# Kernel tuning notes

Hardware: AMD Instinct MI355X
Metric: run time of the kernel (lower is better)

## Reference

```python
import jax, jax.numpy as jnp
import numpy as np
from functools import partial

H = 51

def lstm_cell(x, h, c, W_ih, W_hh, b_ih, b_hh):
    # PyTorch LSTMCell: gates ordered (i, f, g, o)
    z = x @ W_ih.T + b_ih + h @ W_hh.T + b_hh  # [B, 4H]
    i, f, g, o = jnp.split(z, 4, axis=-1)
    i = jax.nn.sigmoid(i)
    f = jax.nn.sigmoid(f)
    g = jnp.tanh(g)
    o = jax.nn.sigmoid(o)
    c_new = f * c + i * g
    h_new = o * jnp.tanh(c_new)
    return h_new, c_new


def setup_inputs() -> dict:
    key = jax.random.key(0)
    ks = jax.random.split(key, 12)
    B, T = 2048, 512
    s = 1.0 / np.sqrt(H)  # PyTorch default init scale
    inp = {
        "input": jax.random.normal(ks[0], (B, T), dtype=jnp.float32),
        "W_ih1": jax.random.uniform(ks[1], (4 * H, 1), jnp.float32, -s, s),
        "W_hh1": jax.random.uniform(ks[2], (4 * H, H), jnp.float32, -s, s),
        "b_ih1": jax.random.uniform(ks[3], (4 * H,), jnp.float32, -s, s),
        "b_hh1": jax.random.uniform(ks[4], (4 * H,), jnp.float32, -s, s),
        "W_ih2": jax.random.uniform(ks[5], (4 * H, H), jnp.float32, -s, s),
        "W_hh2": jax.random.uniform(ks[6], (4 * H, H), jnp.float32, -s, s),
        "b_ih2": jax.random.uniform(ks[7], (4 * H,), jnp.float32, -s, s),
        "b_hh2": jax.random.uniform(ks[8], (4 * H,), jnp.float32, -s, s),
        "W_lin": jax.random.uniform(ks[9], (1, H), jnp.float32, -s, s),
        "b_lin": jax.random.uniform(ks[10], (1,), jnp.float32, -s, s),
        "future": 32,
    }
    return inp


def reference(input, W_ih1, W_hh1, b_ih1, b_hh1, W_ih2, W_hh2, b_ih2, b_hh2, W_lin, b_lin, future):
    B, T = input.shape
    dt = input.dtype
    h1 = jnp.zeros((B, H), dt)
    c1 = jnp.zeros((B, H), dt)
    h2 = jnp.zeros((B, H), dt)
    c2 = jnp.zeros((B, H), dt)

    def core(carry, x_t):
        h1, c1, h2, c2 = carry
        h1, c1 = lstm_cell(x_t, h1, c1, W_ih1, W_hh1, b_ih1, b_hh1)
        h2, c2 = lstm_cell(h1, h2, c2, W_ih2, W_hh2, b_ih2, b_hh2)
        out = h2 @ W_lin.T + b_lin  # [B, 1]
        return (h1, c1, h2, c2), out

    xs = input.T[:, :, None]  # [T, B, 1]
    carry, outs = jax.lax.scan(core, (h1, c1, h2, c2), xs)

    def fstep(carry, _):
        state, out = carry
        new_state, new_out = core(state, out)
        return (new_state, new_out), new_out

    last_out = outs[-1]
    _, fouts = jax.lax.scan(fstep, (carry, last_out), None, length=future)

    all_outs = jnp.concatenate([outs, fouts], axis=0)  # [T+future, B, 1]
    return all_outs[:, :, 0].T  # [B, T+future]
```

## Files before the change

### kernel.cpp

```cpp
#include <hip/hip_runtime.h>

#define H 51
#define TIN 512
#define TTOT 544
#define BTILE 8
#define AST 88
#define H2ST 13
#define SOST 548
#define NTHR 768
#define NSLOT 3

typedef __attribute__((ext_vector_type(8))) short short8;
typedef __attribute__((ext_vector_type(4))) float float4v;

#define MFMA __builtin_amdgcn_mfma_f32_16x16x32_bf16

__device__ __forceinline__ float fast_rcp(float x) { return __builtin_amdgcn_rcpf(x); }
__device__ __forceinline__ float sigf(float x)  { return fast_rcp(1.0f + __expf(-x)); }
__device__ __forceinline__ float tanhf_(float x){ return 1.0f - 2.0f * fast_rcp(1.0f + __expf(2.0f * x)); }

__device__ __forceinline__ unsigned short bf16rnd(float x) {
    unsigned int u = __float_as_uint(x);
    return (unsigned short)((u + 0x7fffu + ((u >> 16) & 1u)) >> 16);
}
__device__ __forceinline__ unsigned int bf16pk(float a, float b) {
    unsigned int r;
    asm("v_cvt_pk_bf16_f32 %0, %1, %2" : "=v"(r) : "v"(a), "v"(b));
    return r;
}
__device__ __forceinline__ void bf16split(float x, unsigned short& hi, float& lo) {
    unsigned int u  = __float_as_uint(x);
    unsigned int hr = (u + 0x7fffu + ((u >> 16) & 1u)) & 0xffff0000u;
    hi = (unsigned short)(hr >> 16);
    lo = x - __uint_as_float(hr);
}

__device__ __forceinline__ float b1val(int k, int u, int g,
                                       const float* Whh1, const float* Wih1) {
    if (u >= H) return 0.0f;
    const int r = g * H + u;
    if (k < H)  return Whh1[r * H + k];
    if (k == H) return Wih1[r];
    return 0.0f;
}
__device__ __forceinline__ float b2val(int k, int u, int g,
                                       const float* Wih2, const float* Whh2) {
    if (u >= H) return 0.0f;
    const int r = g * H + u;
    if (k < H) return Wih2[r * H + k];
    if (k >= 64 && k < 64 + H) return Whh2[r * H + (k - 64)];
    return 0.0f;
}

__global__ __launch_bounds__(NTHR)
__attribute__((amdgpu_waves_per_eu(3, 3)))
void lstm_seq(
    const float* __restrict__ input,
    const float* __restrict__ W_ih1,
    const float* __restrict__ W_hh1,
    const float* __restrict__ b_ih1,
    const float* __restrict__ b_hh1,
    const float* __restrict__ W_ih2,
    const float* __restrict__ W_hh2,
    const float* __restrict__ b_ih2,
    const float* __restrict__ b_hh2,
    const float* __restrict__ W_lin,
    const float* __restrict__ b_lin,
    float* __restrict__ out)
{
    __shared__ __align__(16) unsigned short sA1h[NSLOT][16][AST];
    __shared__ __align__(16) unsigned short sA2h[NSLOT][16][AST];
    __shared__ float sH2f[NSLOT][64][H2ST];
    __shared__ __align__(8) float sXlo[NSLOT][8];
    __shared__ float sWlin[64];
    __shared__ __align__(16) float sIn[BTILE][TIN];
    __shared__ __align__(16) float sOut[BTILE][SOST];
    __shared__ int sCnt[4];

    const int tid  = threadIdx.x;
    const int lane = tid & 63;
    const int wv   = tid >> 6;
    const int ut   = wv & 3;
    const int quad = lane >> 4;
    const int kq   = quad * 8;
    const int nl   = lane & 15;
    const int u    = ut * 16 + nl;
    const int ur   = (u < H) ? u : (H - 1);
    const int b0   = blockIdx.x * BTILE;
    const float blin = b_lin[0];
    const int rowA = (quad & 1) * 4 + (quad >> 1) * 2;
    const int arow = quad * 4;
    const int kc   = lane & 31;
    const int bhead= 2 * ut + (lane >> 5);

    volatile int* vc = (volatile int*)sCnt;
    auto spin = [&](int idx, int v) __attribute__((always_inline)) {
        while (vc[idx] < v) __builtin_amdgcn_s_sleep(1);
        asm volatile("" ::: "memory");
    };
    auto bump = [&](int idx) __attribute__((always_inline)) {
        asm volatile("s_waitcnt lgkmcnt(0)" ::: "memory");
        if (lane == 0) atomicAdd(&sCnt[idx], 1);
    };

    {
        unsigned short* p0 = &sA1h[0][0][0];
        unsigned short* p2 = &sA2h[0][0][0];
        for (int i = tid; i < NSLOT * 16 * AST; i += NTHR) { p0[i] = 0; p2[i] = 0; }
        float* pf = &sH2f[0][0][0];
        for (int i = tid; i < NSLOT * 64 * H2ST; i += NTHR) pf[i] = 0.0f;
        if (tid < NSLOT * 8) sXlo[tid >> 3][tid & 7] = 0.0f;
        if (tid < 64) sWlin[tid] = (tid < H) ? W_lin[tid] : 0.0f;
        if (tid == 0) { sCnt[0] = 0; sCnt[1] = 4; sCnt[2] = 0; }
        for (int i = tid; i < BTILE * (TIN / 4); i += NTHR) {
            const int r = i >> 7, c = i & 127;
            *(float4v*)&sIn[r][c * 4] =
                *(const float4v*)&input[(size_t)(b0 + r) * TIN + c * 4];
        }
    }
    __syncthreads();
    if (tid < 8) {
        unsigned short hh; float lo;
        bf16split(sIn[tid][0], hh, lo);
        sA1h[0][(tid & 2) ? tid + 6 : tid][51] = hh;
        sXlo[0][tid] = lo;
    }
    __syncthreads();

    if (wv < 4) {
        short8 B1h[4][2];
        float zb1[4], wxf[4];
        #pragma unroll
        for (int g = 0; g < 4; ++g) {
            #pragma unroll
            for (int kt = 0; kt < 2; ++kt)
                #pragma unroll
                for (int j = 0; j < 8; ++j)
                    B1h[g][kt][j] = (short)bf16rnd(b1val(kt * 32 + kq + j, u, g, W_hh1, W_ih1));
            const int r = g * H + ur;
            zb1[g] = b_ih1[r] + b_hh1[r];
            wxf[g] = W_ih1[r];
        }
        float c1[2] = {0, 0};

        auto l1work = [&](int rs, int ws) __attribute__((always_inline)) {
            short8 a0h = *(const short8*)&sA1h[rs][nl][kq];
            short8 a1h = *(const short8*)&sA1h[rs][nl][32 + kq];
            float2 xl = *(const float2*)&sXlo[rs][rowA];
            float4v C[4];
            #pragma unroll
            for (int g = 0; g < 4; ++g) {
                float4v c = {zb1[g], zb1[g], zb1[g], zb1[g]};
                c = MFMA(a0h, B1h[g][0], c, 0, 0, 0);
                c = MFMA(a1h, B1h[g][1], c, 0, 0, 0);
                C[g] = c;
            }
            float h1v[2];
            #pragma unroll
            for (int j = 0; j < 2; ++j) {
                const float xr = j ? xl.y : xl.x;
                float I = sigf  (C[0][j] + wxf[0] * xr);
                float F = sigf  (C[1][j] + wxf[1] * xr);
                float G = tanhf_(C[2][j] + wxf[2] * xr);
                float O = sigf  (C[3][j] + wxf[3] * xr);
                c1[j] = F * c1[j] + I * G;
                h1v[j] = O * tanhf_(c1[j]);
            }
            if (u < H) {
                const unsigned int pk = bf16pk(h1v[0], h1v[1]);
                sA1h[ws][arow][u]     = (unsigned short)pk;
                sA1h[ws][arow + 1][u] = (unsigned short)(pk >> 16);
            }
        };

        {
            int si = 0, so = 1, t1 = 0;
            for (int s = 0; s < TIN; ++s) {
                spin(0, t1); spin(2, t1); spin(1, t1 - 4);
                l1work(si, so);
                bump(0);
                t1 += 4;
                si = so; so = (so == 2) ? 0 : so + 1;
            }
        }
        __syncthreads();
        for (int s = TIN; s <= TTOT; ++s) {
            const int rs = s % 3, ws = (s + 1) % 3;
            __syncthreads();
            __syncthreads();
            if (s < TTOT) l1work(rs, ws);
            __syncthreads();
        }
    } else if (wv < 8) {
        short8 B2h[4][4];
        float zb2[4];
        #pragma unroll
        for (int g = 0; g < 4; ++g) {
            #pragma unroll
            for (int kt = 0; kt < 4; ++kt)
                #pragma unroll
                for (int j = 0; j < 8; ++j)
                    B2h[g][kt][j] = (short)bf16rnd(b2val(kt * 32 + kq + j, u, g, W_ih2, W_hh2));
            const int r = g * H + ur;
            zb2[g] = b_ih2[r] + b_hh2[r];
        }
        float c2[2] = {0, 0};

        auto l2work = [&](int rs, int ws) __attribute__((always_inline)) {
            short8 f0h = *(const short8*)&sA1h[rs][nl][kq];
            short8 f1h = *(const short8*)&sA1h[rs][nl][32 + kq];
            short8 f2h = *(const short8*)&sA2h[rs][nl][kq];
            short8 f3h = *(const short8*)&sA2h[rs][nl][32 + kq];
            float4v C[4];
            #pragma unroll
            for (int g = 0; g < 4; ++g) {
                float4v c = {zb2[g], zb2[g], zb2[g], zb2[g]};
                c = MFMA(f0h, B2h[g][0], c, 0, 0, 0);
                c = MFMA(f1h, B2h[g][1], c, 0, 0, 0);
                c = MFMA(f2h, B2h[g][2], c, 0, 0, 0);
                c = MFMA(f3h, B2h[g][3], c, 0, 0, 0);
                C[g] = c;
            }
            float h2v[2];
            #pragma unroll
            for (int j = 0; j < 2; ++j) {
                float I = sigf  (C[0][j]);
                float F = sigf  (C[1][j]);
                float G = tanhf_(C[2][j]);
                float O = sigf  (C[3][j]);
                c2[j] = F * c2[j] + I * G;
                h2v[j] = O * tanhf_(c2[j]);
            }
            if (u < H) {
                const unsigned int pk = bf16pk(h2v[0], h2v[1]);
                sA2h[ws][arow][u]     = (unsigned short)pk;
                sA2h[ws][arow + 1][u] = (unsigned short)(pk >> 16);
                sH2f[rs][u][rowA]     = h2v[0];
                sH2f[rs][u][rowA + 1] = h2v[1];
            }
        };

        {
            int si = 1, so = 2, t4 = 4;
            for (int t = 1; t < TIN; ++t) {
                spin(0, t4); spin(1, t4); spin(2, t4 - 4);
                l2work(si, so);
                bump(1);
                t4 += 4;
                si = so; so = (so == 2) ? 0 : so + 1;
            }
        }
        __syncthreads();
        for (int s = TIN; s <= TTOT; ++s) {
            const int rs = s % 3, ws = (s + 1) % 3;
            l2work(rs, ws);
            __syncthreads();
            __syncthreads();
            __syncthreads();
        }
    } else {
        auto headw = [&](int slot, int outt) __attribute__((always_inline)) -> float {
            float p = sWlin[kc]      * sH2f[slot][kc][bhead]
                    + sWlin[kc + 32] * sH2f[slot][kc + 32][bhead];
            p += __shfl_xor(p, 1);  p += __shfl_xor(p, 2);  p += __shfl_xor(p, 4);
            p += __shfl_xor(p, 8);  p += __shfl_xor(p, 16);
            float val = p + blin;
            if (kc == 0) sOut[bhead][outt] = val;
            return val;
        };

        {
            int sm1 = 2, so = 1, t4 = 0;
            for (int s = 0; s < TIN; ++s) {
                spin(0, t4 - 4);
                if (s >= 2) { spin(1, t4); headw(sm1, s - 2); }
                if ((wv == 8) && (lane < 8) && (s + 1 < TIN)) {
                    unsigned short hh; float lo; bf16split(sIn[lane][s + 1], hh, lo);
                    sA1h[so][(lane & 2) ? lane + 6 : lane][51] = hh;
                    sXlo[so][lane] = lo;
                }
                bump(2);
                t4 += 4;
                sm1 = (sm1 == 2) ? 0 : sm1 + 1;
                so  = (so  == 2) ? 0 : so + 1;
            }
        }
        __syncthreads();
        for (int s = TIN; s <= TTOT; ++s) {
            const int rs = s % 3;
            __syncthreads();
            {
                float val = headw(rs, s - 1);
                if (kc == 0 && s < TTOT) {
                    unsigned short hh; float lo; bf16split(val, hh, lo);
                    sA1h[rs][(bhead & 2) ? bhead + 6 : bhead][51] = hh;
                    sXlo[rs][bhead] = lo;
                }
                if (s == TIN) headw((TIN - 1) % 3, s - 2);
            }
            __syncthreads();
            __syncthreads();
        }
    }

    __syncthreads();
    for (int i = tid; i < BTILE * (TTOT / 4); i += NTHR) {
        const int r = i / (TTOT / 4);
        const int c = i - r * (TTOT / 4);
        *(float4v*)&out[(size_t)(b0 + r) * TTOT + c * 4] =
            *(const float4v*)&sOut[r][c * 4];
    }
}

extern "C" void kernel_launch(void* const* d_in, const int* in_sizes, int n_in,
                              void* d_out, int out_size, void* d_ws, size_t ws_size,
                              hipStream_t stream) {
    const float* input = (const float*)d_in[0];
    const float* W_ih1 = (const float*)d_in[1];
    const float* W_hh1 = (const float*)d_in[2];
    const float* b_ih1 = (const float*)d_in[3];
    const float* b_hh1 = (const float*)d_in[4];
    const float* W_ih2 = (const float*)d_in[5];
    const float* W_hh2 = (const float*)d_in[6];
    const float* b_ih2 = (const float*)d_in[7];
    const float* b_hh2 = (const float*)d_in[8];
    const float* W_lin = (const float*)d_in[9];
    const float* b_lin = (const float*)d_in[10];
    float* out = (float*)d_out;

    lstm_seq<<<dim3(256), dim3(NTHR), 0, stream>>>(input, W_ih1, W_hh1, b_ih1, b_hh1,
                                                   W_ih2, W_hh2, b_ih2, b_hh2,
                                                   W_lin, b_lin, out);
}
```

Baseline: 469.8 us.

## Replace barrier-driven future phase with counter spin-waits and combined three-counter polling

The future-prediction phase (autoregressive steps after the input sequence) now uses the same shared-memory counter handshake as the main loop instead of three or four __syncthreads per step. The slot rotation and counter thresholds are reworked so all three wave groups (layer 1, layer 2, head) proceed in a pipelined fashion throughout. The per-counter spin with s_sleep is replaced by one loop that polls all three counters without sleeping. This cuts barrier overhead and wakeup latency, at the cost of busier polling that competes for LDS bandwidth and issue slots, and a higher risk of ordering bugs in the reworked slot and threshold logic.

```diff
diff --git a/kernel.cpp b/kernel.cpp
--- a/kernel.cpp
+++ b/kernel.cpp
@@ -94,8 +94,11 @@
     const int bhead= 2 * ut + (lane >> 5);
 
     volatile int* vc = (volatile int*)sCnt;
-    auto spin = [&](int idx, int v) __attribute__((always_inline)) {
-        while (vc[idx] < v) __builtin_amdgcn_s_sleep(1);
+    auto spin3 = [&](int v1, int v2, int vA) __attribute__((always_inline)) {
+        for (;;) {
+            int a = vc[0], b = vc[1], c = vc[2];
+            if (a >= v1 && b >= v2 && c >= vA) break;
+        }
         asm volatile("" ::: "memory");
     };
     auto bump = [&](int idx) __attribute__((always_inline)) {
@@ -111,7 +114,7 @@
         for (int i = tid; i < NSLOT * 64 * H2ST; i += NTHR) pf[i] = 0.0f;
         if (tid < NSLOT * 8) sXlo[tid >> 3][tid & 7] = 0.0f;
         if (tid < 64) sWlin[tid] = (tid < H) ? W_lin[tid] : 0.0f;
-        if (tid == 0) { sCnt[0] = 0; sCnt[1] = 4; sCnt[2] = 0; }
+        if (tid == 0) { sCnt[0] = 0; sCnt[1] = 0; sCnt[2] = 0; }
         for (int i = tid; i < BTILE * (TIN / 4); i += NTHR) {
             const int r = i >> 7, c = i & 127;
             *(float4v*)&sIn[r][c * 4] =
@@ -122,8 +125,8 @@
     if (tid < 8) {
         unsigned short hh; float lo;
         bf16split(sIn[tid][0], hh, lo);
-        sA1h[0][(tid & 2) ? tid + 6 : tid][51] = hh;
-        sXlo[0][tid] = lo;
+        sA1h[2][(tid & 2) ? tid + 6 : tid][51] = hh;
+        sXlo[2][tid] = lo;
     }
     __syncthreads();
 
@@ -174,22 +177,21 @@
         };
 
         {
-            int si = 0, so = 1, t1 = 0;
+            int rs = 2, ws = 0;
             for (int s = 0; s < TIN; ++s) {
-                spin(0, t1); spin(2, t1); spin(1, t1 - 4);
-                l1work(si, so);
+                const int t4 = 4 * s;
+                spin3(t4, t4 - 8, t4);
+                l1work(rs, ws);
                 bump(0);
-                t1 += 4;
-                si = so; so = (so == 2) ? 0 : so + 1;
-            }
-        }
-        __syncthreads();
-        for (int s = TIN; s <= TTOT; ++s) {
-            const int rs = s % 3, ws = (s + 1) % 3;
-            __syncthreads();
-            __syncthreads();
-            if (s < TTOT) l1work(rs, ws);
-            __syncthreads();
+                rs = ws; ws = (ws == 2) ? 0 : ws + 1;
+            }
+            for (int s = TIN; s < TTOT; ++s) {
+                const int t4 = 4 * s;
+                spin3(t4, t4 - 8, t4 + 4);
+                l1work(rs, ws);
+                bump(0);
+                rs = ws; ws = (ws == 2) ? 0 : ws + 1;
+            }
         }
     } else if (wv < 8) {
         short8 B2h[4][4];
@@ -235,28 +237,27 @@
                 const unsigned int pk = bf16pk(h2v[0], h2v[1]);
                 sA2h[ws][arow][u]     = (unsigned short)pk;
                 sA2h[ws][arow + 1][u] = (unsigned short)(pk >> 16);
-                sH2f[rs][u][rowA]     = h2v[0];
-                sH2f[rs][u][rowA + 1] = h2v[1];
+                sH2f[ws][u][rowA]     = h2v[0];
+                sH2f[ws][u][rowA + 1] = h2v[1];
             }
         };
 
         {
-            int si = 1, so = 2, t4 = 4;
-            for (int t = 1; t < TIN; ++t) {
-                spin(0, t4); spin(1, t4); spin(2, t4 - 4);
-                l2work(si, so);
+            int rs = 0, ws = 1;
+            for (int k = 1; k < TIN; ++k) {
+                const int t4 = 4 * k;
+                spin3(t4, t4 - 4, t4);
+                l2work(rs, ws);
                 bump(1);
-                t4 += 4;
-                si = so; so = (so == 2) ? 0 : so + 1;
-            }
-        }
-        __syncthreads();
-        for (int s = TIN; s <= TTOT; ++s) {
-            const int rs = s % 3, ws = (s + 1) % 3;
-            l2work(rs, ws);
-            __syncthreads();
-            __syncthreads();
-            __syncthreads();
+                rs = ws; ws = (ws == 2) ? 0 : ws + 1;
+            }
+            for (int k = TIN; k <= TTOT; ++k) {
+                const int t4 = 4 * k;
+                spin3(t4, t4 - 4, t4);
+                l2work(rs, ws);
+                bump(1);
+                rs = ws; ws = (ws == 2) ? 0 : ws + 1;
+            }
         }
     } else {
         auto headw = [&](int slot, int outt) __attribute__((always_inline)) -> float {
@@ -270,36 +271,36 @@
         };
 
         {
-            int sm1 = 2, so = 1, t4 = 0;
+            int hs = 2, ss = 0;
             for (int s = 0; s < TIN; ++s) {
-                spin(0, t4 - 4);
-                if (s >= 2) { spin(1, t4); headw(sm1, s - 2); }
+                const int t4 = 4 * s;
+                spin3(t4 - 4, t4 - 4, t4);
+                if (s >= 2) headw(hs, s - 2);
                 if ((wv == 8) && (lane < 8) && (s + 1 < TIN)) {
                     unsigned short hh; float lo; bf16split(sIn[lane][s + 1], hh, lo);
-                    sA1h[so][(lane & 2) ? lane + 6 : lane][51] = hh;
-                    sXlo[so][lane] = lo;
+                    sA1h[ss][(lane & 2) ? lane + 6 : lane][51] = hh;
+                    sXlo[ss][lane] = lo;
                 }
                 bump(2);
-                t4 += 4;
-                sm1 = (sm1 == 2) ? 0 : sm1 + 1;
-                so  = (so  == 2) ? 0 : so + 1;
-            }
-        }
-        __syncthreads();
-        for (int s = TIN; s <= TTOT; ++s) {
-            const int rs = s % 3;
-            __syncthreads();
-            {
-                float val = headw(rs, s - 1);
-                if (kc == 0 && s < TTOT) {
-                    unsigned short hh; float lo; bf16split(val, hh, lo);
-                    sA1h[rs][(bhead & 2) ? bhead + 6 : bhead][51] = hh;
-                    sXlo[rs][bhead] = lo;
+                hs = (hs == 2) ? 0 : hs + 1;
+                ss = (ss == 2) ? 0 : ss + 1;
+            }
+            for (int s = TIN; s <= TTOT; ++s) {
+                const int t4 = 4 * s;
+                spin3(t4 - 8, t4, t4);
+                const int hsl = s % 3;
+                const int xsl = (s + 2) % 3;
+                {
+                    float val = headw(hsl, s - 1);
+                    if (kc == 0 && s < TTOT) {
+                        unsigned short hh; float lo; bf16split(val, hh, lo);
+                        sA1h[xsl][(bhead & 2) ? bhead + 6 : bhead][51] = hh;
+                        sXlo[xsl][bhead] = lo;
+                    }
+                    if (s == TIN) headw((TIN - 1) % 3, TIN - 2);
                 }
-                if (s == TIN) headw((TIN - 1) % 3, s - 2);
-            }
-            __syncthreads();
-            __syncthreads();
+                bump(2);
+            }
         }
     }
 
```

Result: no change. 475.6 us (+1.2%).
